# Optimization experiments

Measured on AMD Instinct MI355X. Metric: run time of the kernel, lower is better.

Reference implementation:

```python
import jax, jax.numpy as jnp
import numpy as np

K = 3          # kernel_size
G = 8          # group
C = 256        # in_channel
EPS_BN = 1e-5
EPS_SGE = 1e-5


def setup_inputs() -> dict:
    key = jax.random.key(0)
    ks = jax.random.split(key, 6)
    x = jax.random.normal(ks[0], (8, C, 96, 96), dtype=jnp.float32)
    fan_out = (G * K * K) * K * K  # out_channels * kh * kw (kaiming fan_out)
    conv_weight = jax.random.normal(ks[1], (G * K * K, C, K, K), dtype=jnp.float32) * np.float32(np.sqrt(2.0 / fan_out))
    bn_gamma = 1.0 + 0.1 * jax.random.normal(ks[2], (G * K * K,), dtype=jnp.float32)
    bn_beta = 0.1 * jax.random.normal(ks[3], (G * K * K,), dtype=jnp.float32)
    sge_weight = 0.1 * jax.random.normal(ks[4], (1, G, 1, 1), dtype=jnp.float32)
    sge_bias = 1.0 + 0.1 * jax.random.normal(ks[5], (1, G, 1, 1), dtype=jnp.float32)
    return {"x": x, "sge_weight": sge_weight, "sge_bias": sge_bias,
            "conv_weight": conv_weight, "bn_gamma": bn_gamma, "bn_beta": bn_beta}


def _reflect_pad(x, p):
    return jnp.pad(x, ((0, 0), (0, 0), (p, p), (p, p)), mode="reflect")


def _sge(x, weight, bias):
    # SpatialGroupEnhance
    b, c, h, w = x.shape
    xg = x.reshape(b * G, c // G, h, w)
    gap = xg.mean(axis=(2, 3), keepdims=True)        # AdaptiveAvgPool2d(1)
    xn = (xg * gap).sum(axis=1, keepdims=True)       # (b*G,1,h,w)
    t = xn.reshape(b * G, h * w)
    t = t - t.mean(axis=1, keepdims=True)
    std = jnp.std(t, axis=1, ddof=1, keepdims=True) + EPS_SGE  # torch .std() is unbiased
    t = (t / std).reshape(b, G, h, w)
    t = t * weight + bias
    gate = jax.nn.sigmoid(t.reshape(b * G, 1, h, w))
    return (xg * gate).reshape(b, c, h, w)


def _pasa(x, conv_weight, bn_gamma, bn_beta):
    # Downsample_PASA_group_softmax (stride=1)
    n, c, h, w = x.shape
    xp = _reflect_pad(x, K // 2)
    s = jax.lax.conv_general_dilated(xp, conv_weight, (1, 1), "VALID",
                                     dimension_numbers=("NCHW", "OIHW", "NCHW"))
    # BatchNorm2d in training mode: batch statistics over (N,H,W), biased var
    mean = s.mean(axis=(0, 2, 3))
    var = s.var(axis=(0, 2, 3))
    s = (s - mean[None, :, None, None]) * jax.lax.rsqrt(var + EPS_BN)[None, :, None, None]
    s = s * bn_gamma[None, :, None, None] + bn_beta[None, :, None, None]
    s = jax.nn.softmax(s, axis=1)                    # over the G*K*K channels
    # channels are (group, k*k) group-major -> (n, G, 1, K*K, H*W)
    return s.reshape(n, G, K * K, h * w)[:, :, None, :, :]


def _unfold(xp, h, w):
    # xp already padded; returns (b, c, K*K, h, w) with torch F.unfold ordering
    return jnp.stack([xp[:, :, i:i + h, j:j + w]
                      for i in range(K) for j in range(K)], axis=2)


def reference(x, sge_weight, sge_bias, conv_weight, bn_gamma, bn_beta):
    n, c, h, w = x.shape
    sigma = _pasa(x, conv_weight, bn_gamma, bn_beta)       # (n, G, 1, KK, HW)
    xe = _sge(x, sge_weight, sge_bias)
    patches = _unfold(_reflect_pad(xe, K // 2), h, w)      # (n, c, KK, h, w)
    patches = patches.reshape(n, G, c // G, K * K, h * w)  # split c group-major
    out = (patches * sigma).sum(axis=3)                    # reduce over K*K taps
    return out.reshape(n, c, h, w)
```

## Files before the change

### kernel.cpp

```cpp
#include <hip/hip_runtime.h>
#include <hip/hip_bf16.h>

#define B_  8
#define C_  256
#define H_  96
#define W_  96
#define G_  8
#define CPG 32
#define KK  9
#define O_  72
#define HW  9216
#define NPX 73728

typedef short bf16x8 __attribute__((ext_vector_type(8)));
typedef float f32x4 __attribute__((ext_vector_type(4)));

__device__ __forceinline__ unsigned short f2bf(float f) {
    union { float f; unsigned u; } v; v.f = f;
    unsigned r = v.u + 0x7fffu + ((v.u >> 16) & 1u);
    return (unsigned short)(r >> 16);
}
__device__ __forceinline__ float bf2f(unsigned short h) {
    union { float f; unsigned u; } v; v.u = ((unsigned)h) << 16;
    return v.f;
}

__global__ __launch_bounds__(256) void bprep_kernel(const float* __restrict__ w,
                                                    unsigned short* __restrict__ bpk) {
    int idx = blockIdx.x * 256 + threadIdx.x;
    if (idx >= 368640) return;
    int tix2 = idx / 5120;
    int r = idx - tix2 * 5120;
    int fi = r >> 9;
    int p = fi / 5, nt = fi - p * 5;
    int li = r & 511;
    int l = li >> 3, j = li & 7;
    int tap = tix2 >> 3, cblk = tix2 & 7;
    int o = nt * 16 + (l & 15);
    int c = cblk * 32 + ((l >> 4) << 3) + j;
    unsigned short val = 0;
    if (o < O_) {
        float wv = w[((size_t)o * C_ + c) * KK + tap];
        unsigned short h = f2bf(wv);
        val = (p == 0) ? h : f2bf(wv - bf2f(h));
    }
    bpk[idx] = val;
}

__global__ __launch_bounds__(256) void gap_kernel(const float* __restrict__ x,
                                                  float* __restrict__ gap) {
    int bc = blockIdx.x;
    const float4* p = (const float4*)(x + (size_t)bc * HW);
    float sum = 0.f;
    for (int idx = threadIdx.x; idx < HW / 4; idx += 256) {
        float4 v = p[idx];
        sum += v.x + v.y + v.z + v.w;
    }
    #pragma unroll
    for (int m = 32; m >= 1; m >>= 1) sum += __shfl_xor(sum, m, 64);
    __shared__ float red[4];
    int wid = threadIdx.x >> 6;
    if ((threadIdx.x & 63) == 0) red[wid] = sum;
    __syncthreads();
    if (threadIdx.x == 0)
        gap[bc] = (red[0] + red[1] + red[2] + red[3]) * (1.f / (float)HW);
}

__global__ __launch_bounds__(256) void xn_kernel(const float* __restrict__ x,
                                                 const float* __restrict__ gap,
                                                 float* __restrict__ xng,
                                                 float* __restrict__ sge_stats) {
    int blk = blockIdx.x;
    int bg = blk / 36, chunk = blk % 36;
    int b = bg >> 3, g = bg & 7;
    int p = chunk * 256 + threadIdx.x;
    const float* xbase = x + ((size_t)b * C_ + g * CPG) * HW + p;
    const float* gp = gap + b * C_ + g * CPG;
    float v = 0.f;
    #pragma unroll
    for (int ch = 0; ch < CPG; ch++) v += xbase[(size_t)ch * HW] * gp[ch];
    xng[(size_t)bg * HW + p] = v;
    float v1 = v, v2 = v * v;
    #pragma unroll
    for (int m = 32; m >= 1; m >>= 1) {
        v1 += __shfl_xor(v1, m, 64);
        v2 += __shfl_xor(v2, m, 64);
    }
    __shared__ float r1[4], r2[4];
    int wid = threadIdx.x >> 6;
    if ((threadIdx.x & 63) == 0) { r1[wid] = v1; r2[wid] = v2; }
    __syncthreads();
    if (threadIdx.x == 0) {
        atomicAdd(&sge_stats[bg * 2 + 0], r1[0] + r1[1] + r1[2] + r1[3]);
        atomicAdd(&sge_stats[bg * 2 + 1], r2[0] + r2[1] + r2[2] + r2[3]);
    }
}

__global__ __launch_bounds__(256) void gate_kernel(float* __restrict__ xng,
                                                   const float* __restrict__ stats,
                                                   const float* __restrict__ sw,
                                                   const float* __restrict__ sb) {
    int idx = blockIdx.x * 256 + threadIdx.x;
    int bg = idx / HW;
    int g = bg & 7;
    float sum = stats[bg * 2], sumsq = stats[bg * 2 + 1];
    float mean = sum * (1.f / (float)HW);
    float var = (sumsq - sum * mean) * (1.f / (float)(HW - 1));
    var = fmaxf(var, 0.f);
    float sd = sqrtf(var) + 1e-5f;
    float tv = (xng[idx] - mean) / sd * sw[g] + sb[g];
    xng[idx] = 1.f / (1.f + expf(-tv));
}

#define STAGE_LOAD(CH) do {                                                      \
    const float* p0_ = sb0 + (size_t)(CH) * 32 * HW;                             \
    const float* p1_ = p0_ + HW;                                                 \
    _Pragma("unroll")                                                            \
    for (int m2 = 0; m2 < 6; m2++) {                                             \
        a0[m2] = *(const f32x4*)(p0_ + 4 * m2);                                  \
        a1[m2] = *(const f32x4*)(p1_ + 4 * m2);                                  \
    }                                                                            \
} while (0)

#define PACK_HL(F0, F1, HI, LO) do {                                             \
    unsigned b0_ = __builtin_bit_cast(unsigned, (F0));                           \
    unsigned b1_ = __builtin_bit_cast(unsigned, (F1));                           \
    HI = __builtin_amdgcn_perm(b1_, b0_, 0x07060302u);                           \
    float h0_ = __builtin_bit_cast(float, b0_ & 0xffff0000u);                    \
    float h1_ = __builtin_bit_cast(float, b1_ & 0xffff0000u);                    \
    LO = __builtin_amdgcn_perm(__builtin_bit_cast(unsigned, (F1) - h1_),         \
                               __builtin_bit_cast(unsigned, (F0) - h0_),         \
                               0x07060302u);                                     \
} while (0)

#define STAGE_WRITE() do {                                                       \
    _Pragma("unroll")                                                            \
    for (int m2 = 0; m2 < 6; m2++)                                               \
        _Pragma("unroll")                                                        \
        for (int e = 0; e < 4; e++) {                                            \
            int col = sq * 24 + 1 + m2 * 4 + e;                                  \
            unsigned hi_, lo_;                                                   \
            PACK_HL(a0[m2][e], a1[m2][e], hi_, lo_);                             \
            int row = (rbase + col) ^ par;                                       \
            int off = row * 16 + ((spHi ^ ((col >> 1) & 3)) << 2) + spLo;        \
            xsH[off] = hi_; xsL[off] = lo_;                                      \
        }                                                                        \
    if (sq == 0 || sq == 3) {                                                    \
        float f0_ = (sq == 0) ? a0[0][1] : a0[5][2];                             \
        float f1_ = (sq == 0) ? a1[0][1] : a1[5][2];                             \
        int col = (sq == 0) ? 0 : 97;                                            \
        unsigned hi_, lo_;                                                       \
        PACK_HL(f0_, f1_, hi_, lo_);                                             \
        int row = (rbase + col) ^ par;                                           \
        int off = row * 16 + ((spHi ^ ((col >> 1) & 3)) << 2) + spLo;            \
        xsH[off] = hi_; xsL[off] = lo_;                                          \
    }                                                                            \
} while (0)

__global__ __launch_bounds__(256, 2) void conv_kernel(const float* __restrict__ x,
                                                      const unsigned short* __restrict__ bpk,
                                                      float* __restrict__ sA,
                                                      float* __restrict__ sB) {
    __shared__ unsigned xsH[4 * 98 * 16];
    __shared__ unsigned xsL[4 * 98 * 16];
    __shared__ f32x4 blsv[2][640];
    int phys = blockIdx.x;
    int blk = (phys & 7) * 96 + (phys >> 3);
    int kh = blk & 1;
    int np = blk >> 1;
    int n = np / 48, pair = np % 48;
    int i0 = pair * 2;
    int t = threadIdx.x;
    int l = t & 63, wave = t >> 6;
    int rw = wave & 1, mh = wave >> 1;
    int l15 = l & 15, lg = l >> 4;
    int colb = mh * 48 + l15;
    int khb = kh * 4;
    const float* xb = x + (size_t)n * C_ * HW + (size_t)kh * 128 * HW;
    float* sOut = kh ? sB : sA;

    int sp = t & 15, srr = (t >> 4) & 3, sq = wave;
    int sri = i0 - 1 + srr;
    if (sri < 0) sri = 1; else if (sri > 95) sri = 94;
    const float* sb0 = xb + (size_t)(2 * sp) * HW + sri * W_ + sq * 24;
    int spHi = sp >> 2, spLo = sp & 3;
    int rbase = srr * 98, par = srr & 1;

    f32x4 acc[3][5];
    #pragma unroll
    for (int m = 0; m < 3; m++)
        #pragma unroll
        for (int nt = 0; nt < 5; nt++)
            #pragma unroll
            for (int e = 0; e < 4; e++) acc[m][nt][e] = 0.f;

    f32x4 a0[6], a1[6];

    {
        const f32x4* srcB = (const f32x4*)(bpk + (size_t)khb * 5120);
        f32x4 b0 = srcB[t], b1 = srcB[t + 256], b2;
        if (t < 128) b2 = srcB[t + 512];
        blsv[0][t] = b0; blsv[0][t + 256] = b1;
        if (t < 128) blsv[0][t + 512] = b2;
        STAGE_LOAD(0);
        STAGE_WRITE();
    }
    __syncthreads();

    for (int ch = 0; ch < 4; ch++) {
        #pragma unroll 1
        for (int tap = 0; tap < 9; tap++) {
            int g = ch * 9 + tap;
            int buf = g & 1;
            int dr = tap / 3, dc = tap - dr * 3;
            const unsigned short* bb = (const unsigned short*)&blsv[buf][0];
            bf16x8 bh[5], blo[5];
            #pragma unroll
            for (int nt = 0; nt < 5; nt++) {
                bh[nt]  = *(const bf16x8*)(bb + nt * 512 + (l << 3));
                blo[nt] = *(const bf16x8*)(bb + (5 + nt) * 512 + (l << 3));
            }
            int rr = rw + dr;
            int rpar = rr & 1, rb = rr * 98;
            int cs = ((colb + dc) >> 1) & 3;
            int sl = (lg ^ cs) << 2;
            bf16x8 ah[3], al[3];
            #pragma unroll
            for (int m = 0; m < 3; m++) {
                int row = (rb + colb + m * 16 + dc) ^ rpar;
                ah[m] = *(const bf16x8*)&xsH[row * 16 + sl];
                al[m] = *(const bf16x8*)&xsL[row * 16 + sl];
            }
            f32x4 pb0, pb1, pb2;
            bool hasNext = (g < 35);
            if (hasNext) {
                int tix2n = (tap < 8) ? (tap + 1) * 8 + khb + ch : khb + ch + 1;
                const f32x4* srcB = (const f32x4*)(bpk + (size_t)tix2n * 5120);
                pb0 = srcB[t]; pb1 = srcB[t + 256];
                if (t < 128) pb2 = srcB[t + 512];
            }
            if (tap == 7 && ch < 3) STAGE_LOAD(ch + 1);
            #pragma unroll
            for (int m = 0; m < 3; m++)
                #pragma unroll
                for (int nt = 0; nt < 5; nt++) {
                    acc[m][nt] = __builtin_amdgcn_mfma_f32_16x16x32_bf16(ah[m], bh[nt],  acc[m][nt], 0, 0, 0);
                    acc[m][nt] = __builtin_amdgcn_mfma_f32_16x16x32_bf16(ah[m], blo[nt], acc[m][nt], 0, 0, 0);
                    acc[m][nt] = __builtin_amdgcn_mfma_f32_16x16x32_bf16(al[m], bh[nt],  acc[m][nt], 0, 0, 0);
                }
            if (hasNext) {
                blsv[buf ^ 1][t] = pb0; blsv[buf ^ 1][t + 256] = pb1;
                if (t < 128) blsv[buf ^ 1][t + 512] = pb2;
                __syncthreads();
            }
        }
        if (ch < 3) {
            STAGE_WRITE();
            __syncthreads();
        }
    }

    int i = i0 + rw;
    #pragma unroll
    for (int nt = 0; nt < 5; nt++) {
        int o = nt * 16 + l15;
        if (o < O_) {
            #pragma unroll
            for (int m = 0; m < 3; m++) {
                int px = mh * 48 + m * 16 + (lg << 2);
                *(f32x4*)(sOut + ((size_t)(n * O_ + o) * H_ + i) * W_ + px) = acc[m][nt];
            }
        }
    }
}

__global__ __launch_bounds__(256) void bnstats_kernel(float* __restrict__ sA,
                                                      const float* __restrict__ sB,
                                                      float* __restrict__ bn_stats) {
    int blk = blockIdx.x;
    int o = blk / B_, nn = blk % B_;
    size_t base = ((size_t)nn * O_ + o) * HW;
    f32x4* pa = (f32x4*)(sA + base);
    const f32x4* pb = (const f32x4*)(sB + base);
    float s1 = 0.f, s2 = 0.f;
    for (int idx = threadIdx.x; idx < HW / 4; idx += 256) {
        f32x4 v = pa[idx] + pb[idx];
        pa[idx] = v;
        s1 += v[0] + v[1] + v[2] + v[3];
        s2 += v[0] * v[0] + v[1] * v[1] + v[2] * v[2] + v[3] * v[3];
    }
    #pragma unroll
    for (int m = 32; m >= 1; m >>= 1) {
        s1 += __shfl_xor(s1, m, 64);
        s2 += __shfl_xor(s2, m, 64);
    }
    __shared__ float r1[4], r2[4];
    int wid = threadIdx.x >> 6;
    if ((threadIdx.x & 63) == 0) { r1[wid] = s1; r2[wid] = s2; }
    __syncthreads();
    if (threadIdx.x == 0) {
        atomicAdd(&bn_stats[o * 2 + 0], r1[0] + r1[1] + r1[2] + r1[3]);
        atomicAdd(&bn_stats[o * 2 + 1], r2[0] + r2[1] + r2[2] + r2[3]);
    }
}

__global__ __launch_bounds__(256, 2) void out_kernel(const float* __restrict__ x,
                                                     const float* __restrict__ s,
                                                     const float* __restrict__ bn_stats,
                                                     const float* __restrict__ gamma,
                                                     const float* __restrict__ beta,
                                                     const float* __restrict__ gate,
                                                     float* __restrict__ out) {
    int blk = blockIdx.x;
    int n = blk / H_, i = blk % H_;
    int t = threadIdx.x;
    __shared__ float sg[O_][W_];
    __shared__ float rden[W_];
    __shared__ float gt[G_][3][98];

    int r0 = i - 1; if (r0 < 0) r0 = 1;
    int r2 = i + 1; if (r2 > 95) r2 = 94;
    int rows[3] = { r0, i, r2 };

    for (int idx = t; idx < G_ * 3 * 98; idx += 256) {
        int g = idx / (3 * 98), rem = idx % (3 * 98);
        int r = rem / 98, col = rem % 98;
        int gcol = col - 1;
        if (gcol < 0) gcol = 1; else if (gcol > 95) gcol = 94;
        gt[g][r][col] = gate[((size_t)(n * G_ + g)) * HW + rows[r] * W_ + gcol];
    }
    const float inv = 1.f / (float)NPX;
    for (int idx = t; idx < O_ * W_; idx += 256) {
        int o = idx / W_, j = idx % W_;
        float sum = bn_stats[o * 2], ssq = bn_stats[o * 2 + 1];
        float mean = sum * inv;
        float var = ssq * inv - mean * mean;
        float sc = rsqrtf(var + 1e-5f) * gamma[o];
        float val = (s[((size_t)(n * O_ + o) * H_ + i) * W_ + j] - mean) * sc + beta[o];
        sg[o][j] = expf(val);
    }
    __syncthreads();
    if (t < W_) {
        float d = 0.f;
        #pragma unroll
        for (int o = 0; o < O_; o++) d += sg[o][t];
        rden[t] = 1.f / d;
    }
    __syncthreads();

    const float* xb = x + (size_t)n * C_ * HW;
    for (int idx = t; idx < C_ * W_; idx += 256) {
        int c = idx / W_, j = idx % W_;
        int g = c >> 5;
        const float* xc = xb + (size_t)c * HW;
        int jm1 = j - 1; if (jm1 < 0) jm1 = 1;
        int jp1 = j + 1; if (jp1 > 95) jp1 = 94;
        int cols[3] = { jm1, j, jp1 };
        float acc = 0.f;
        #pragma unroll
        for (int r = 0; r < 3; r++) {
            const float* xr = xc + rows[r] * W_;
            #pragma unroll
            for (int dx = 0; dx < 3; dx++) {
                float xv = xr[cols[dx]];
                float gv = gt[g][r][j + dx];
                float sv = sg[g * 9 + r * 3 + dx][j];
                acc += xv * gv * sv;
            }
        }
        out[((size_t)(n * C_ + c) * H_ + i) * W_ + j] = acc * rden[j];
    }
}

extern "C" void kernel_launch(void* const* d_in, const int* in_sizes, int n_in,
                              void* d_out, int out_size, void* d_ws, size_t ws_size,
                              hipStream_t stream) {
    const float* x      = (const float*)d_in[0];
    const float* sge_w  = (const float*)d_in[1];
    const float* sge_b  = (const float*)d_in[2];
    const float* conv_w = (const float*)d_in[3];
    const float* gamma  = (const float*)d_in[4];
    const float* beta   = (const float*)d_in[5];
    float* out = (float*)d_out;
    float* ws = (float*)d_ws;

    float* sge_stats = ws;
    float* bn_stats  = ws + 128;
    float* gap       = ws + 272;
    float* xng       = ws + 2320;
    unsigned short* bpk = (unsigned short*)(ws + 592144);
    float* sA        = ws + 776464;
    float* sB = (float*)d_out;

    hipMemsetAsync(d_ws, 0, 272 * sizeof(float), stream);
    hipLaunchKernelGGL(bprep_kernel,   dim3(1440),        dim3(256), 0, stream, conv_w, bpk);
    hipLaunchKernelGGL(gap_kernel,     dim3(B_ * C_),     dim3(256), 0, stream, x, gap);
    hipLaunchKernelGGL(xn_kernel,      dim3(B_ * G_ * 36),dim3(256), 0, stream, x, gap, xng, sge_stats);
    hipLaunchKernelGGL(gate_kernel,    dim3(B_ * G_ * 36),dim3(256), 0, stream, xng, sge_stats, sge_w, sge_b);
    hipLaunchKernelGGL(conv_kernel,    dim3(768),         dim3(256), 0, stream, x, bpk, sA, sB);
    hipLaunchKernelGGL(bnstats_kernel, dim3(O_ * B_),     dim3(256), 0, stream, sA, sB, bn_stats);
    hipLaunchKernelGGL(out_kernel,     dim3(B_ * H_),     dim3(256), 0, stream, x, sA, bn_stats, gamma, beta, xng, out);
}
```

Measured before the change: 213.2 us.

## Fuse global average pool into conv kernel staging and drop gap kernel

Removes the separate gap_kernel that read all of x once. The conv kernel already stages x rows into LDS, so it now sums the interior rows per channel into shared memory and atomically adds them to a global gap buffer. The 1/HW scaling moves into xn_kernel, and conv now runs before xn so the gap values are ready when xn reads them. This saves a full pass over the 75MB input, at the cost of extra adds and atomics in the conv staging path and a larger memset.

```diff
diff --git a/kernel.cpp b/kernel.cpp
--- a/kernel.cpp
+++ b/kernel.cpp
@@ -47,25 +47,6 @@
     bpk[idx] = val;
 }
 
-__global__ __launch_bounds__(256) void gap_kernel(const float* __restrict__ x,
-                                                  float* __restrict__ gap) {
-    int bc = blockIdx.x;
-    const float4* p = (const float4*)(x + (size_t)bc * HW);
-    float sum = 0.f;
-    for (int idx = threadIdx.x; idx < HW / 4; idx += 256) {
-        float4 v = p[idx];
-        sum += v.x + v.y + v.z + v.w;
-    }
-    #pragma unroll
-    for (int m = 32; m >= 1; m >>= 1) sum += __shfl_xor(sum, m, 64);
-    __shared__ float red[4];
-    int wid = threadIdx.x >> 6;
-    if ((threadIdx.x & 63) == 0) red[wid] = sum;
-    __syncthreads();
-    if (threadIdx.x == 0)
-        gap[bc] = (red[0] + red[1] + red[2] + red[3]) * (1.f / (float)HW);
-}
-
 __global__ __launch_bounds__(256) void xn_kernel(const float* __restrict__ x,
                                                  const float* __restrict__ gap,
                                                  float* __restrict__ xng,
@@ -79,6 +60,7 @@
     float v = 0.f;
     #pragma unroll
     for (int ch = 0; ch < CPG; ch++) v += xbase[(size_t)ch * HW] * gp[ch];
+    v *= (1.f / (float)HW);
     xng[(size_t)bg * HW + p] = v;
     float v1 = v, v2 = v * v;
     #pragma unroll
@@ -133,7 +115,7 @@
                                0x07060302u);                                     \
 } while (0)
 
-#define STAGE_WRITE() do {                                                       \
+#define STAGE_WRITE(CH) do {                                                     \
     _Pragma("unroll")                                                            \
     for (int m2 = 0; m2 < 6; m2++)                                               \
         _Pragma("unroll")                                                        \
@@ -155,15 +137,27 @@
         int off = row * 16 + ((spHi ^ ((col >> 1) & 3)) << 2) + spLo;            \
         xsH[off] = hi_; xsL[off] = lo_;                                          \
     }                                                                            \
+    if (srr == 1 || srr == 2) {         \
+        float s0_ = 0.f, s1_ = 0.f;                                              \
+        _Pragma("unroll")                                                        \
+        for (int m2 = 0; m2 < 6; m2++) {                                         \
+            s0_ += a0[m2][0] + a0[m2][1] + a0[m2][2] + a0[m2][3];                \
+            s1_ += a1[m2][0] + a1[m2][1] + a1[m2][2] + a1[m2][3];                \
+        }                                                                        \
+        atomicAdd(&gapL[(CH) * 32 + 2 * sp],     s0_);                           \
+        atomicAdd(&gapL[(CH) * 32 + 2 * sp + 1], s1_);                           \
+    }                                                                            \
 } while (0)
 
 __global__ __launch_bounds__(256, 2) void conv_kernel(const float* __restrict__ x,
                                                       const unsigned short* __restrict__ bpk,
                                                       float* __restrict__ sA,
-                                                      float* __restrict__ sB) {
+                                                      float* __restrict__ sB,
+                                                      float* __restrict__ gap) {
     __shared__ unsigned xsH[4 * 98 * 16];
     __shared__ unsigned xsL[4 * 98 * 16];
     __shared__ f32x4 blsv[2][640];
+    __shared__ float gapL[128];
     int phys = blockIdx.x;
     int blk = (phys & 7) * 96 + (phys >> 3);
     int kh = blk & 1;
@@ -186,6 +180,9 @@
     int spHi = sp >> 2, spLo = sp & 3;
     int rbase = srr * 98, par = srr & 1;
 
+    if (t < 128) gapL[t] = 0.f;
+    __syncthreads();
+
     f32x4 acc[3][5];
     #pragma unroll
     for (int m = 0; m < 3; m++)
@@ -203,7 +200,7 @@
         blsv[0][t] = b0; blsv[0][t + 256] = b1;
         if (t < 128) blsv[0][t + 512] = b2;
         STAGE_LOAD(0);
-        STAGE_WRITE();
+        STAGE_WRITE(0);
     }
     __syncthreads();
 
@@ -255,7 +252,7 @@
             }
         }
         if (ch < 3) {
-            STAGE_WRITE();
+            STAGE_WRITE(ch + 1);
             __syncthreads();
         }
     }
@@ -272,6 +269,7 @@
             }
         }
     }
+    if (t < 128) atomicAdd(&gap[n * C_ + kh * 128 + t], gapL[t]);
 }
 
 __global__ __launch_bounds__(256) void bnstats_kernel(float* __restrict__ sA,
@@ -392,12 +390,11 @@
     float* sA        = ws + 776464;
     float* sB = (float*)d_out;
 
-    hipMemsetAsync(d_ws, 0, 272 * sizeof(float), stream);
+    hipMemsetAsync(d_ws, 0, 2320 * sizeof(float), stream);
     hipLaunchKernelGGL(bprep_kernel,   dim3(1440),        dim3(256), 0, stream, conv_w, bpk);
-    hipLaunchKernelGGL(gap_kernel,     dim3(B_ * C_),     dim3(256), 0, stream, x, gap);
+    hipLaunchKernelGGL(conv_kernel,    dim3(768),         dim3(256), 0, stream, x, bpk, sA, sB, gap);
     hipLaunchKernelGGL(xn_kernel,      dim3(B_ * G_ * 36),dim3(256), 0, stream, x, gap, xng, sge_stats);
     hipLaunchKernelGGL(gate_kernel,    dim3(B_ * G_ * 36),dim3(256), 0, stream, xng, sge_stats, sge_w, sge_b);
-    hipLaunchKernelGGL(conv_kernel,    dim3(768),         dim3(256), 0, stream, x, bpk, sA, sB);
     hipLaunchKernelGGL(bnstats_kernel, dim3(O_ * B_),     dim3(256), 0, stream, sA, sB, bn_stats);
     hipLaunchKernelGGL(out_kernel,     dim3(B_ * H_),     dim3(256), 0, stream, x, sA, bn_stats, gamma, beta, xng, out);
 }
```

New measurement: 204.6 us. 1.04x faster.
